# Kernel optimization log

Measured on AMD Instinct MI355X. Metric: run time of the kernel, lower is better.

Reference implementation:

```python
import jax, jax.numpy as jnp
import numpy as np

W_CE = 0.1
W_BOUND = 0.1
SMOOTH = 1e-06
IGNORE_INDEX = -100


def _edt_to_seeds(seed):
    """Exact Euclidean distance to nearest True pixel (Felzenszwalb-style separable EDT).

    seed: [H, W] bool. Returns [H, W] float32 distances (0 at seed pixels).
    Equivalent to scipy.ndimage.distance_transform_edt(~seed ... ) semantics:
    distance from every pixel to the nearest seed pixel.
    """
    H, W = seed.shape
    BIG = jnp.float32(H + W)  # upper bound on any in-image distance
    x = jnp.arange(W, dtype=jnp.float32)
    # 1D horizontal distance to nearest seed in the same row
    pos_l = jnp.where(seed, x, jnp.float32(-1e9))
    left = jax.lax.cummax(pos_l, axis=1)
    dl = x - left
    pos_r = jnp.where(seed, x, jnp.float32(1e9))
    right = jax.lax.cummin(pos_r, axis=1, reverse=True)
    dr = right - x
    d1 = jnp.minimum(jnp.minimum(dl, dr), BIG)  # [H, W], capped to avoid overflow
    g2 = d1 * d1  # squared horizontal distances
    # Vertical lower-envelope pass: dist2[y,x] = min_y' (y-y')^2 + g2[y',x]
    y = jnp.arange(H, dtype=jnp.float32)
    diff2 = (y[:, None] - y[None, :]) ** 2  # [H, H]
    dist2 = jnp.min(diff2[:, :, None] + g2[None, :, :], axis=1)  # [H, W]
    return jnp.sqrt(dist2)


def _signed_distance(class_mask):
    """signed = EDT(~mask) - EDT(mask) per scipy convention; 0 if mask empty."""
    has_pos = class_mask.any()
    has_neg = jnp.logical_not(class_mask).any()
    dist_out = _edt_to_seeds(class_mask)            # dist to nearest inside pixel (0 inside)
    dist_in = _edt_to_seeds(jnp.logical_not(class_mask))  # dist to nearest outside pixel (0 outside)
    signed = jnp.where(has_neg, dist_out - dist_in, dist_out)
    return jnp.where(has_pos, signed, jnp.zeros_like(signed))


def _dist_maps(targets, valid, num_classes):
    B, H, W = targets.shape
    t_safe = jnp.where(valid, targets, 0)
    cls = jnp.arange(num_classes, dtype=t_safe.dtype)
    cm = (t_safe[:, None, :, :] == cls[None, :, None, None]) & valid[:, None, :, :]  # [B,C,H,W]
    flat = cm.reshape(B * num_classes, H, W)
    signed = jax.lax.map(_signed_distance, flat).reshape(B, num_classes, H, W)
    return signed * valid[:, None, :, :].astype(jnp.float32)  # zero out invalid pixels


def setup_inputs() -> dict:
    key = jax.random.key(0)
    k1, k2 = jax.random.split(key)
    inputs = jax.random.normal(k1, (4, 8, 256, 256), dtype=jnp.float32)
    targets = jax.random.randint(k2, (4, 256, 256), 0, 8, dtype=jnp.int32)
    return {"inputs": inputs, "targets": targets}


def reference(inputs, targets):
    B, C, H, W = inputs.shape
    logp = jax.nn.log_softmax(inputs, axis=1)
    probs = jnp.exp(logp)
    # CrossEntropyLoss (all targets valid, mean over B*H*W)
    ce = -jnp.mean(jnp.take_along_axis(logp, targets[:, None, :, :].astype(jnp.int32), axis=1))
    # Dice loss (valid mask = targets >= 0)
    valid_d = targets >= 0
    t_safe = jnp.where(valid_d, targets, 0)
    onehot = jax.nn.one_hot(t_safe, C, dtype=jnp.float32).transpose(0, 3, 1, 2)  # [B,C,H,W]
    vm = valid_d[:, None, :, :].astype(jnp.float32)
    ps = probs * vm
    th = onehot * vm
    intersection = jnp.sum(ps * th)
    cardinality = jnp.sum(ps + th)
    dice = 1.0 - (2.0 * intersection + SMOOTH) / (cardinality + SMOOTH)
    dice_total = W_CE * ce + (1.0 - W_CE) * dice  # DiceCELoss.forward
    # Boundary loss (signed distance maps, mean reduction)
    valid_b = (targets != IGNORE_INDEX) & (targets >= 0) & (targets < C)
    dmaps = _dist_maps(targets, valid_b, C)
    vbf = valid_b[:, None, :, :].astype(jnp.float32)
    bound = jnp.sum(probs * dmaps * vbf) / (jnp.sum(vbf) + 1e-08)
    return W_CE * ce + (1.0 - W_CE - W_BOUND) * dice_total + W_BOUND * bound
```

## Files before the change

kernel.cpp:

```cpp
#include <hip/hip_runtime.h>
#include <math.h>

#define B_DIM 4
#define C_DIM 8
#define H_DIM 256
#define W_DIM 256
#define HW 65536
#define NPIX 262144


__device__ __forceinline__ float wave_reduce_f(float v) {
#pragma unroll
    for (int off = 32; off; off >>= 1) v += __shfl_xor(v, off, 64);
    return v;
}

__global__ void __launch_bounds__(256) k_row(
    const float* __restrict__ x, const int* __restrict__ tgt,
    float* __restrict__ lse_out, float* __restrict__ pce, float* __restrict__ pinter,
    int2* __restrict__ pcnt, unsigned long long* __restrict__ wmask_g,
    float* __restrict__ bound_part, unsigned int* __restrict__ cnt,
    unsigned int* __restrict__ gdone) {
    int bi = blockIdx.x;
    int b = bi >> 8, y = bi & 255;
    int i = threadIdx.x;
    int lane = i & 63, wid = i >> 6;
    size_t rowbase = (size_t)b * HW + (size_t)y * W_DIM;

    if (bi == 0) {
        if (i < 32) { bound_part[i << 5] = 0.0f; cnt[i << 5] = 0u; }
        if (i == 32) *gdone = 0u;
    }

    const float* xb = x + (size_t)b * C_DIM * HW + (size_t)y * W_DIM + i;
    float v[C_DIM];
    float m = -1e30f;
#pragma unroll
    for (int c = 0; c < C_DIM; ++c) { v[c] = xb[(size_t)c * HW]; m = fmaxf(m, v[c]); }
    float s = 0.f;
#pragma unroll
    for (int c = 0; c < C_DIM; ++c) s += __expf(v[c] - m);
    float lse = m + __logf(s);
    lse_out[rowbase + i] = lse;

    int t = tgt[rowbase + i];
    bool valid_d = (t >= 0);
    bool valid_b = valid_d && (t < C_DIM);
    int tc = valid_b ? t : 0;
    float vt = v[0];
#pragma unroll
    for (int c = 1; c < C_DIM; ++c) vt = (tc == c) ? v[c] : vt;

    float ce = lse - vt;
    float inter = valid_b ? __expf(vt - lse) : 0.f;

    __shared__ float ws_ce[4], ws_in[4];
    __shared__ int ws_cd[4], ws_cb[4];
    float r_ce = wave_reduce_f(ce);
    float r_in = wave_reduce_f(inter);
    unsigned long long md = __ballot(valid_d);
    unsigned long long mbv = __ballot(valid_b);
    if (lane == 0) {
        ws_ce[wid] = r_ce; ws_in[wid] = r_in;
        ws_cd[wid] = __popcll(md); ws_cb[wid] = __popcll(mbv);
    }

    __shared__ unsigned long long wmask[C_DIM][4];
#pragma unroll
    for (int c = 0; c < C_DIM; ++c) {
        unsigned long long mc = __ballot(valid_b && (t == c));
        if (lane == 0) wmask[c][wid] = mc;
    }
    __syncthreads();

    if (i == 0) {
        pce[bi] = (ws_ce[0] + ws_ce[1]) + (ws_ce[2] + ws_ce[3]);
        pinter[bi] = (ws_in[0] + ws_in[1]) + (ws_in[2] + ws_in[3]);
        pcnt[bi] = make_int2((ws_cd[0] + ws_cd[1]) + (ws_cd[2] + ws_cd[3]),
                             (ws_cb[0] + ws_cb[1]) + (ws_cb[2] + ws_cb[3]));
    }
    if (i < 32) {
        int c = i >> 2, w = i & 3;
        wmask_g[((size_t)((b * C_DIM + c) * 256 + y) << 2) + w] = wmask[c][w];
    }
}

#define LDS_PITCH 20
#define ENVELOPE(H, MA, MB)                                                     \
    {                                                                           \
        float4 qa0 = *(const float4*)&H[ybase][tx << 2];                        \
        float4 qb0 = *(const float4*)&H[ybase + 1][tx << 2];                    \
        MA.x = fminf(qa0.x, qb0.x + 1.0f); MB.x = fminf(qb0.x, qa0.x + 1.0f);   \
        MA.y = fminf(qa0.y, qb0.y + 1.0f); MB.y = fminf(qb0.y, qa0.y + 1.0f);   \
        MA.z = fminf(qa0.z, qb0.z + 1.0f); MB.z = fminf(qb0.z, qa0.z + 1.0f);   \
        MA.w = fminf(qa0.w, qb0.w + 1.0f); MB.w = fminf(qb0.w, qa0.w + 1.0f);   \
        int s = 1;                                                              \
        for (;;) {                                                              \
            int ra = max(ybase - s, 0);                                         \
            int rb = min(ybase + 1 + s, H_DIM - 1);                             \
            float4 qa = *(const float4*)&H[ra][tx << 2];                        \
            float4 qb = *(const float4*)&H[rb][tx << 2];                        \
            float s2a = (float)(s * s);                                         \
            float s2b = (float)((s + 1) * (s + 1));                             \
            MA.x = fminf(MA.x, fminf(qa.x + s2a, qb.x + s2b));                  \
            MA.y = fminf(MA.y, fminf(qa.y + s2a, qb.y + s2b));                  \
            MA.z = fminf(MA.z, fminf(qa.z + s2a, qb.z + s2b));                  \
            MA.w = fminf(MA.w, fminf(qa.w + s2a, qb.w + s2b));                  \
            MB.x = fminf(MB.x, fminf(qa.x + s2b, qb.x + s2a));                  \
            MB.y = fminf(MB.y, fminf(qa.y + s2b, qb.y + s2a));                  \
            MB.z = fminf(MB.z, fminf(qa.z + s2b, qb.z + s2a));                  \
            MB.w = fminf(MB.w, fminf(qa.w + s2b, qb.w + s2a));                  \
            float lmax = fmaxf(fmaxf(fmaxf(MA.x, MA.y), fmaxf(MA.z, MA.w)),     \
                               fmaxf(fmaxf(MB.x, MB.y), fmaxf(MB.z, MB.w)));    \
            ++s;                                                                \
            float st = (float)(s * s);                                          \
            if (s >= H_DIM || __all(st >= lmax)) break;                         \
        }                                                                       \
    }

__global__ void __launch_bounds__(512) k_cols(
    const unsigned long long* __restrict__ wmask_g, const float* __restrict__ x,
    const float* __restrict__ lse, const int* __restrict__ tgt,
    const float* __restrict__ pce, const float* __restrict__ pinter,
    const int2* __restrict__ pcnt,
    float* __restrict__ bound_part, unsigned int* __restrict__ cnt,
    unsigned int* __restrict__ gdone, float* __restrict__ out) {
    int blk = blockIdx.x;
    int bc = blk >> 4;
    int xt = blk & 15;
    int b = bc >> 3, c = bc & 7;
    int tid = threadIdx.x;
    int tx = tid & 3;
    int ybase = (tid >> 2) << 1;
    int lane = tid & 63, wid = tid >> 6;

    __shared__ float h0s[H_DIM][LDS_PITCH];
    __shared__ float h1s[H_DIM][LDS_PITCH];
    __shared__ int anyf[2];
    __shared__ float wsum[8];
    __shared__ int sh_last;
    __shared__ double dred[512];

    size_t pixbase = (size_t)b * HW;
    size_t xplane = ((size_t)b * C_DIM + c) * HW;
    int x0 = (xt << 4) + (tx << 2);
    size_t row0 = (size_t)ybase * W_DIM + x0;
    size_t row1 = row0 + W_DIM;
    float4 xv0 = *(const float4*)(x + xplane + row0);
    float4 xv1 = *(const float4*)(x + xplane + row1);
    float4 lv0 = *(const float4*)(lse + pixbase + row0);
    float4 lv1 = *(const float4*)(lse + pixbase + row1);
    int4 tv0 = *(const int4*)(tgt + pixbase + row0);
    int4 tv1 = *(const int4*)(tgt + pixbase + row1);

    int srow = tid & 255;
    int pol = tid >> 8;
    const unsigned long long* mrow = wmask_g + ((size_t)(bc * 256 + srow) << 2);
    unsigned long long w0 = mrow[0], w1 = mrow[1], w2 = mrow[2], w3 = mrow[3];

    if (tid < 2) anyf[tid] = 0;
    __syncthreads();
    if (pol == 0) {
        unsigned long long orv = w0 | w1 | w2 | w3;
        unsigned long long bp = __ballot(orv != 0ull);
        if (lane == 0 && bp) atomicOr(&anyf[0], 1);
    } else {
        unsigned long long andv = w0 & w1 & w2 & w3;
        unsigned long long bn = __ballot(andv != ~0ull);
        if (lane == 0 && bn) atomicOr(&anyf[1], 1);
    }

    {
        unsigned long long q0 = pol ? ~w0 : w0;
        unsigned long long q1 = pol ? ~w1 : w1;
        unsigned long long q2 = pol ? ~w2 : w2;
        unsigned long long q3 = pol ? ~w3 : w3;
        int wi = xt >> 2;
        int b0base = (xt & 3) << 4;
        int gc0 = xt << 4;
        int wbase = wi << 6;
        int h0p = q0 ? (63 - __builtin_clzll(q0)) : -100000;
        int h1p = q1 ? (127 - __builtin_clzll(q1)) : h0p;
        int h2p = q2 ? (191 - __builtin_clzll(q2)) : h1p;
        int lastp = (wi == 0) ? -100000 : (wi == 1) ? h0p : (wi == 2) ? h1p : h2p;
        int l3p = q3 ? (192 + __builtin_ctzll(q3)) : 100000;
        int l2p = q2 ? (128 + __builtin_ctzll(q2)) : l3p;
        int l1p = q1 ? (64 + __builtin_ctzll(q1)) : l2p;
        int nextp = (wi == 0) ? l1p : (wi == 1) ? l2p : (wi == 2) ? l3p : 100000;
        unsigned long long wn = (wi == 0) ? q0 : (wi == 1) ? q1 : (wi == 2) ? q2 : q3;
        unsigned long long lowmask = (b0base == 0) ? 0ull : ((~0ull) >> (64 - b0base));
        unsigned long long wlow = wn & lowmask;
        int lastw = wlow ? (wbase + 63 - __builtin_clzll(wlow)) : lastp;
        int hib = b0base + 16;
        unsigned long long whigh = (hib == 64) ? 0ull : (wn & ((~0ull) << hib));
        int nextw = whigh ? (wbase + __builtin_ctzll(whigh)) : nextp;
        unsigned int wseg = (unsigned int)((wn >> b0base) & 0xFFFFull);

        int d1l[16], d1r[16];
        int dl = gc0 - lastw;
#pragma unroll
        for (int i2 = 0; i2 < 16; ++i2) {
            dl = ((wseg >> i2) & 1u) ? 0 : dl;
            d1l[i2] = dl;
            ++dl;
        }
        int dr = nextw - (gc0 + 15);
#pragma unroll
        for (int i2 = 15; i2 >= 0; --i2) {
            dr = ((wseg >> i2) & 1u) ? 0 : dr;
            d1r[i2] = dr;
            ++dr;
        }
        float fd[16];
#pragma unroll
        for (int i2 = 0; i2 < 16; ++i2) {
            int d1 = min(min(d1l[i2], d1r[i2]), 512);
            fd[i2] = (float)d1 * (float)d1;
        }
        float (*hp)[LDS_PITCH] = pol ? h1s : h0s;
        *(float4*)&hp[srow][0]  = make_float4(fd[0], fd[1], fd[2], fd[3]);
        *(float4*)&hp[srow][4]  = make_float4(fd[4], fd[5], fd[6], fd[7]);
        *(float4*)&hp[srow][8]  = make_float4(fd[8], fd[9], fd[10], fd[11]);
        *(float4*)&hp[srow][12] = make_float4(fd[12], fd[13], fd[14], fd[15]);
    }
    __syncthreads();

    float4 m0a, m0b, m1a, m1b;
    ENVELOPE(h0s, m0a, m0b)
    ENVELOPE(h1s, m1a, m1b)

    bool has_pos = anyf[0] != 0;
    bool has_neg = anyf[1] != 0;

    float lsum = 0.f;
#pragma unroll
    for (int iy = 0; iy < 2; ++iy) {
        float4 M0 = iy ? m0b : m0a;
        float4 M1 = iy ? m1b : m1a;
        float4 xv = iy ? xv1 : xv0;
        float4 lv = iy ? lv1 : lv0;
        int4 tv = iy ? tv1 : tv0;
#pragma unroll
        for (int j = 0; j < 4; ++j) {
            float d2o = (j == 0) ? M0.x : (j == 1) ? M0.y : (j == 2) ? M0.z : M0.w;
            float d2i = (j == 0) ? M1.x : (j == 1) ? M1.y : (j == 2) ? M1.z : M1.w;
            float dout = sqrtf(d2o), din = sqrtf(d2i);
            float sgn = has_pos ? (has_neg ? (dout - din) : dout) : 0.f;
            float xs = (j == 0) ? xv.x : (j == 1) ? xv.y : (j == 2) ? xv.z : xv.w;
            float ls = (j == 0) ? lv.x : (j == 1) ? lv.y : (j == 2) ? lv.z : lv.w;
            int tt   = (j == 0) ? tv.x : (j == 1) ? tv.y : (j == 2) ? tv.z : tv.w;
            bool vb = (tt >= 0) && (tt < C_DIM);
            float prob = __expf(xs - ls);
            lsum += vb ? prob * sgn : 0.f;
        }
    }

    float r2 = wave_reduce_f(lsum);
    if (lane == 0) wsum[wid] = r2;
    __syncthreads();
    if (tid == 0) {
        float bsum = ((wsum[0] + wsum[1]) + (wsum[2] + wsum[3]))
                   + ((wsum[4] + wsum[5]) + (wsum[6] + wsum[7]));
        float old = atomicAdd(&bound_part[bc << 5], bsum);
        asm volatile("" :: "v"(old));
        unsigned int o = atomicAdd(&cnt[bc << 5], 1u);
        int lastflag = 0;
        if (o == 15u) {
            unsigned int g = atomicAdd(gdone, 1u);
            lastflag = (g == 31u) ? 1 : 0;
        }
        sh_last = lastflag;
    }
    __syncthreads();
    if (!sh_last) return;

    double s_ce = 0, s_in = 0, c_d = 0, c_b = 0;
    for (int k = tid; k < 1024; k += 512) {
        s_ce += (double)pce[k]; s_in += (double)pinter[k];
        int2 cc = pcnt[k]; c_d += (double)cc.x; c_b += (double)cc.y;
    }
    double sums[3]; double vin[3] = {s_ce, s_in, c_d * 4194304.0 + c_b};
    for (int q = 0; q < 3; ++q) {
        dred[tid] = vin[q];
        __syncthreads();
        for (int s2 = 256; s2; s2 >>= 1) { if (tid < s2) dred[tid] += dred[tid + s2]; __syncthreads(); }
        sums[q] = dred[0];
        __syncthreads();
    }
    __shared__ float bpart_s[32];
    if (tid < 32) bpart_s[tid] = atomicAdd(&bound_part[tid << 5], 0.0f);
    __syncthreads();
    if (tid == 0) {
        double btot = 0.0;
        for (int k = 0; k < 32; ++k) btot += (double)bpart_s[k];
        double packed = sums[2];
        double cd = floor(packed / 4194304.0 + 1e-9);
        double cb = packed - cd * 4194304.0;
        double ce = sums[0] / (double)NPIX;
        double inter = sums[1];
        double card = cd + cb;
        double dice = 1.0 - (2.0 * inter + 1e-6) / (card + 1e-6);
        double dice_total = 0.1 * ce + 0.9 * dice;
        double bound = btot / (cb + 1e-8);
        out[0] = (float)(0.1 * ce + 0.8 * dice_total + 0.1 * bound);
    }
}

extern "C" void kernel_launch(void* const* d_in, const int* in_sizes, int n_in,
                              void* d_out, int out_size, void* d_ws, size_t ws_size,
                              hipStream_t stream) {
    const float* x = (const float*)d_in[0];
    const int* tgt = (const int*)d_in[1];
    float* out = (float*)d_out;

    char* ws = (char*)d_ws;
    float* pce    = (float*)(ws + 0);
    float* pinter = (float*)(ws + 4096);
    int2*  pcnt   = (int2*)(ws + 8192);
    float* bound_part = (float*)(ws + 16384);
    unsigned int* cnt = (unsigned int*)(ws + 20480);
    unsigned int* gdone = (unsigned int*)(ws + 24576);
    float* lse    = (float*)(ws + 65536);
    unsigned long long* wmask_g = (unsigned long long*)(ws + (size_t)(2u << 20));

    k_row<<<1024, 256, 0, stream>>>(x, tgt, lse, pce, pinter, pcnt, wmask_g,
                                    bound_part, cnt, gdone);
    k_cols<<<512, 512, 0, stream>>>(wmask_g, x, lse, tgt, pce, pinter, pcnt,
                                    bound_part, cnt, gdone, out);
}
```

Baseline: 22.14 us.

## Narrow k_cols column tiles to 8 and fuse both EDT polarities per thread

k_cols now launches 1024 blocks of 256 threads, each covering 8 columns instead of 16. Each thread computes both the inside and outside horizontal distance rows, and the vertical envelope loop processes both polarities together with one shared early-exit vote. The aim is more blocks for better CU coverage and a single fused loop instead of two sequential envelope passes. The trade-off is that the fused loop runs to the slower polarity's termination, and per-block setup, mask loads and atomics are doubled.

```diff
diff --git a/kernel.cpp b/kernel.cpp
--- a/kernel.cpp
+++ b/kernel.cpp
@@ -85,40 +85,8 @@
     }
 }
 
-#define LDS_PITCH 20
-#define ENVELOPE(H, MA, MB)                                                     \
-    {                                                                           \
-        float4 qa0 = *(const float4*)&H[ybase][tx << 2];                        \
-        float4 qb0 = *(const float4*)&H[ybase + 1][tx << 2];                    \
-        MA.x = fminf(qa0.x, qb0.x + 1.0f); MB.x = fminf(qb0.x, qa0.x + 1.0f);   \
-        MA.y = fminf(qa0.y, qb0.y + 1.0f); MB.y = fminf(qb0.y, qa0.y + 1.0f);   \
-        MA.z = fminf(qa0.z, qb0.z + 1.0f); MB.z = fminf(qb0.z, qa0.z + 1.0f);   \
-        MA.w = fminf(qa0.w, qb0.w + 1.0f); MB.w = fminf(qb0.w, qa0.w + 1.0f);   \
-        int s = 1;                                                              \
-        for (;;) {                                                              \
-            int ra = max(ybase - s, 0);                                         \
-            int rb = min(ybase + 1 + s, H_DIM - 1);                             \
-            float4 qa = *(const float4*)&H[ra][tx << 2];                        \
-            float4 qb = *(const float4*)&H[rb][tx << 2];                        \
-            float s2a = (float)(s * s);                                         \
-            float s2b = (float)((s + 1) * (s + 1));                             \
-            MA.x = fminf(MA.x, fminf(qa.x + s2a, qb.x + s2b));                  \
-            MA.y = fminf(MA.y, fminf(qa.y + s2a, qb.y + s2b));                  \
-            MA.z = fminf(MA.z, fminf(qa.z + s2a, qb.z + s2b));                  \
-            MA.w = fminf(MA.w, fminf(qa.w + s2a, qb.w + s2b));                  \
-            MB.x = fminf(MB.x, fminf(qa.x + s2b, qb.x + s2a));                  \
-            MB.y = fminf(MB.y, fminf(qa.y + s2b, qb.y + s2a));                  \
-            MB.z = fminf(MB.z, fminf(qa.z + s2b, qb.z + s2a));                  \
-            MB.w = fminf(MB.w, fminf(qa.w + s2b, qb.w + s2a));                  \
-            float lmax = fmaxf(fmaxf(fmaxf(MA.x, MA.y), fmaxf(MA.z, MA.w)),     \
-                               fmaxf(fmaxf(MB.x, MB.y), fmaxf(MB.z, MB.w)));    \
-            ++s;                                                                \
-            float st = (float)(s * s);                                          \
-            if (s >= H_DIM || __all(st >= lmax)) break;                         \
-        }                                                                       \
-    }
-
-__global__ void __launch_bounds__(512) k_cols(
+#define LDS_PITCH 12
+__global__ void __launch_bounds__(256) k_cols(
     const unsigned long long* __restrict__ wmask_g, const float* __restrict__ x,
     const float* __restrict__ lse, const int* __restrict__ tgt,
     const float* __restrict__ pce, const float* __restrict__ pinter,
@@ -126,24 +94,24 @@
     float* __restrict__ bound_part, unsigned int* __restrict__ cnt,
     unsigned int* __restrict__ gdone, float* __restrict__ out) {
     int blk = blockIdx.x;
-    int bc = blk >> 4;
-    int xt = blk & 15;
+    int bc = blk >> 5;
+    int x8 = blk & 31;
     int b = bc >> 3, c = bc & 7;
     int tid = threadIdx.x;
-    int tx = tid & 3;
-    int ybase = (tid >> 2) << 1;
+    int tx = tid & 1;
+    int ybase = (tid >> 1) << 1;
     int lane = tid & 63, wid = tid >> 6;
 
     __shared__ float h0s[H_DIM][LDS_PITCH];
     __shared__ float h1s[H_DIM][LDS_PITCH];
     __shared__ int anyf[2];
-    __shared__ float wsum[8];
+    __shared__ float wsum[4];
     __shared__ int sh_last;
-    __shared__ double dred[512];
+    __shared__ double dred[256];
 
     size_t pixbase = (size_t)b * HW;
     size_t xplane = ((size_t)b * C_DIM + c) * HW;
-    int x0 = (xt << 4) + (tx << 2);
+    int x0 = (x8 << 3) + (tx << 2);
     size_t row0 = (size_t)ybase * W_DIM + x0;
     size_t row1 = row0 + W_DIM;
     float4 xv0 = *(const float4*)(x + xplane + row0);
@@ -153,81 +121,129 @@
     int4 tv0 = *(const int4*)(tgt + pixbase + row0);
     int4 tv1 = *(const int4*)(tgt + pixbase + row1);
 
-    int srow = tid & 255;
-    int pol = tid >> 8;
-    const unsigned long long* mrow = wmask_g + ((size_t)(bc * 256 + srow) << 2);
+    const unsigned long long* mrow = wmask_g + ((size_t)(bc * 256 + tid) << 2);
     unsigned long long w0 = mrow[0], w1 = mrow[1], w2 = mrow[2], w3 = mrow[3];
 
     if (tid < 2) anyf[tid] = 0;
     __syncthreads();
-    if (pol == 0) {
+    {
         unsigned long long orv = w0 | w1 | w2 | w3;
+        unsigned long long andv = w0 & w1 & w2 & w3;
         unsigned long long bp = __ballot(orv != 0ull);
-        if (lane == 0 && bp) atomicOr(&anyf[0], 1);
-    } else {
-        unsigned long long andv = w0 & w1 & w2 & w3;
         unsigned long long bn = __ballot(andv != ~0ull);
-        if (lane == 0 && bn) atomicOr(&anyf[1], 1);
+        if (lane == 0) {
+            if (bp) atomicOr(&anyf[0], 1);
+            if (bn) atomicOr(&anyf[1], 1);
+        }
     }
 
     {
-        unsigned long long q0 = pol ? ~w0 : w0;
-        unsigned long long q1 = pol ? ~w1 : w1;
-        unsigned long long q2 = pol ? ~w2 : w2;
-        unsigned long long q3 = pol ? ~w3 : w3;
-        int wi = xt >> 2;
-        int b0base = (xt & 3) << 4;
-        int gc0 = xt << 4;
+        int wi = x8 >> 3;
+        int b0base = (x8 & 7) << 3;
+        int gc0 = x8 << 3;
         int wbase = wi << 6;
-        int h0p = q0 ? (63 - __builtin_clzll(q0)) : -100000;
-        int h1p = q1 ? (127 - __builtin_clzll(q1)) : h0p;
-        int h2p = q2 ? (191 - __builtin_clzll(q2)) : h1p;
-        int lastp = (wi == 0) ? -100000 : (wi == 1) ? h0p : (wi == 2) ? h1p : h2p;
-        int l3p = q3 ? (192 + __builtin_ctzll(q3)) : 100000;
-        int l2p = q2 ? (128 + __builtin_ctzll(q2)) : l3p;
-        int l1p = q1 ? (64 + __builtin_ctzll(q1)) : l2p;
-        int nextp = (wi == 0) ? l1p : (wi == 1) ? l2p : (wi == 2) ? l3p : 100000;
-        unsigned long long wn = (wi == 0) ? q0 : (wi == 1) ? q1 : (wi == 2) ? q2 : q3;
-        unsigned long long lowmask = (b0base == 0) ? 0ull : ((~0ull) >> (64 - b0base));
-        unsigned long long wlow = wn & lowmask;
-        int lastw = wlow ? (wbase + 63 - __builtin_clzll(wlow)) : lastp;
-        int hib = b0base + 16;
-        unsigned long long whigh = (hib == 64) ? 0ull : (wn & ((~0ull) << hib));
-        int nextw = whigh ? (wbase + __builtin_ctzll(whigh)) : nextp;
-        unsigned int wseg = (unsigned int)((wn >> b0base) & 0xFFFFull);
-
-        int d1l[16], d1r[16];
-        int dl = gc0 - lastw;
-#pragma unroll
-        for (int i2 = 0; i2 < 16; ++i2) {
-            dl = ((wseg >> i2) & 1u) ? 0 : dl;
-            d1l[i2] = dl;
-            ++dl;
-        }
-        int dr = nextw - (gc0 + 15);
-#pragma unroll
-        for (int i2 = 15; i2 >= 0; --i2) {
-            dr = ((wseg >> i2) & 1u) ? 0 : dr;
-            d1r[i2] = dr;
-            ++dr;
-        }
-        float fd[16];
-#pragma unroll
-        for (int i2 = 0; i2 < 16; ++i2) {
-            int d1 = min(min(d1l[i2], d1r[i2]), 512);
-            fd[i2] = (float)d1 * (float)d1;
-        }
-        float (*hp)[LDS_PITCH] = pol ? h1s : h0s;
-        *(float4*)&hp[srow][0]  = make_float4(fd[0], fd[1], fd[2], fd[3]);
-        *(float4*)&hp[srow][4]  = make_float4(fd[4], fd[5], fd[6], fd[7]);
-        *(float4*)&hp[srow][8]  = make_float4(fd[8], fd[9], fd[10], fd[11]);
-        *(float4*)&hp[srow][12] = make_float4(fd[12], fd[13], fd[14], fd[15]);
+#pragma unroll
+        for (int pol = 0; pol < 2; ++pol) {
+            unsigned long long q0 = pol ? ~w0 : w0;
+            unsigned long long q1 = pol ? ~w1 : w1;
+            unsigned long long q2 = pol ? ~w2 : w2;
+            unsigned long long q3 = pol ? ~w3 : w3;
+            int h0p = q0 ? (63 - __builtin_clzll(q0)) : -100000;
+            int h1p = q1 ? (127 - __builtin_clzll(q1)) : h0p;
+            int h2p = q2 ? (191 - __builtin_clzll(q2)) : h1p;
+            int lastp = (wi == 0) ? -100000 : (wi == 1) ? h0p : (wi == 2) ? h1p : h2p;
+            int l3p = q3 ? (192 + __builtin_ctzll(q3)) : 100000;
+            int l2p = q2 ? (128 + __builtin_ctzll(q2)) : l3p;
+            int l1p = q1 ? (64 + __builtin_ctzll(q1)) : l2p;
+            int nextp = (wi == 0) ? l1p : (wi == 1) ? l2p : (wi == 2) ? l3p : 100000;
+            unsigned long long wn = (wi == 0) ? q0 : (wi == 1) ? q1 : (wi == 2) ? q2 : q3;
+            unsigned long long lowmask = (b0base == 0) ? 0ull : ((~0ull) >> (64 - b0base));
+            unsigned long long wlow = wn & lowmask;
+            int lastw = wlow ? (wbase + 63 - __builtin_clzll(wlow)) : lastp;
+            int hib = b0base + 8;
+            unsigned long long whigh = (hib == 64) ? 0ull : (wn & ((~0ull) << hib));
+            int nextw = whigh ? (wbase + __builtin_ctzll(whigh)) : nextp;
+            unsigned int wseg = (unsigned int)((wn >> b0base) & 0xFFull);
+
+            int d1l[8], d1r[8];
+            int dl = gc0 - lastw;
+#pragma unroll
+            for (int i2 = 0; i2 < 8; ++i2) {
+                dl = ((wseg >> i2) & 1u) ? 0 : dl;
+                d1l[i2] = dl;
+                ++dl;
+            }
+            int dr = nextw - (gc0 + 7);
+#pragma unroll
+            for (int i2 = 7; i2 >= 0; --i2) {
+                dr = ((wseg >> i2) & 1u) ? 0 : dr;
+                d1r[i2] = dr;
+                ++dr;
+            }
+            float fd[8];
+#pragma unroll
+            for (int i2 = 0; i2 < 8; ++i2) {
+                int d1 = min(min(d1l[i2], d1r[i2]), 512);
+                fd[i2] = (float)d1 * (float)d1;
+            }
+            float (*hp)[LDS_PITCH] = pol ? h1s : h0s;
+            *(float4*)&hp[tid][0] = make_float4(fd[0], fd[1], fd[2], fd[3]);
+            *(float4*)&hp[tid][4] = make_float4(fd[4], fd[5], fd[6], fd[7]);
+        }
     }
     __syncthreads();
 
     float4 m0a, m0b, m1a, m1b;
-    ENVELOPE(h0s, m0a, m0b)
-    ENVELOPE(h1s, m1a, m1b)
+    {
+        int col = tx << 2;
+        float4 a0 = *(const float4*)&h0s[ybase][col];
+        float4 b0v = *(const float4*)&h0s[ybase + 1][col];
+        float4 a1 = *(const float4*)&h1s[ybase][col];
+        float4 b1v = *(const float4*)&h1s[ybase + 1][col];
+        m0a.x = fminf(a0.x, b0v.x + 1.0f); m0b.x = fminf(b0v.x, a0.x + 1.0f);
+        m0a.y = fminf(a0.y, b0v.y + 1.0f); m0b.y = fminf(b0v.y, a0.y + 1.0f);
+        m0a.z = fminf(a0.z, b0v.z + 1.0f); m0b.z = fminf(b0v.z, a0.z + 1.0f);
+        m0a.w = fminf(a0.w, b0v.w + 1.0f); m0b.w = fminf(b0v.w, a0.w + 1.0f);
+        m1a.x = fminf(a1.x, b1v.x + 1.0f); m1b.x = fminf(b1v.x, a1.x + 1.0f);
+        m1a.y = fminf(a1.y, b1v.y + 1.0f); m1b.y = fminf(b1v.y, a1.y + 1.0f);
+        m1a.z = fminf(a1.z, b1v.z + 1.0f); m1b.z = fminf(b1v.z, a1.z + 1.0f);
+        m1a.w = fminf(a1.w, b1v.w + 1.0f); m1b.w = fminf(b1v.w, a1.w + 1.0f);
+        int s = 1;
+        for (;;) {
+            int ra = max(ybase - s, 0);
+            int rb = min(ybase + 1 + s, H_DIM - 1);
+            float4 qa0 = *(const float4*)&h0s[ra][col];
+            float4 qb0 = *(const float4*)&h0s[rb][col];
+            float4 qa1 = *(const float4*)&h1s[ra][col];
+            float4 qb1 = *(const float4*)&h1s[rb][col];
+            float s2a = (float)(s * s);
+            float s2b = (float)((s + 1) * (s + 1));
+            m0a.x = fminf(m0a.x, fminf(qa0.x + s2a, qb0.x + s2b));
+            m0a.y = fminf(m0a.y, fminf(qa0.y + s2a, qb0.y + s2b));
+            m0a.z = fminf(m0a.z, fminf(qa0.z + s2a, qb0.z + s2b));
+            m0a.w = fminf(m0a.w, fminf(qa0.w + s2a, qb0.w + s2b));
+            m0b.x = fminf(m0b.x, fminf(qa0.x + s2b, qb0.x + s2a));
+            m0b.y = fminf(m0b.y, fminf(qa0.y + s2b, qb0.y + s2a));
+            m0b.z = fminf(m0b.z, fminf(qa0.z + s2b, qb0.z + s2a));
+            m0b.w = fminf(m0b.w, fminf(qa0.w + s2b, qb0.w + s2a));
+            m1a.x = fminf(m1a.x, fminf(qa1.x + s2a, qb1.x + s2b));
+            m1a.y = fminf(m1a.y, fminf(qa1.y + s2a, qb1.y + s2b));
+            m1a.z = fminf(m1a.z, fminf(qa1.z + s2a, qb1.z + s2b));
+            m1a.w = fminf(m1a.w, fminf(qa1.w + s2a, qb1.w + s2b));
+            m1b.x = fminf(m1b.x, fminf(qa1.x + s2b, qb1.x + s2a));
+            m1b.y = fminf(m1b.y, fminf(qa1.y + s2b, qb1.y + s2a));
+            m1b.z = fminf(m1b.z, fminf(qa1.z + s2b, qb1.z + s2a));
+            m1b.w = fminf(m1b.w, fminf(qa1.w + s2b, qb1.w + s2a));
+            float l0 = fmaxf(fmaxf(fmaxf(m0a.x, m0a.y), fmaxf(m0a.z, m0a.w)),
+                             fmaxf(fmaxf(m0b.x, m0b.y), fmaxf(m0b.z, m0b.w)));
+            float l1 = fmaxf(fmaxf(fmaxf(m1a.x, m1a.y), fmaxf(m1a.z, m1a.w)),
+                             fmaxf(fmaxf(m1b.x, m1b.y), fmaxf(m1b.z, m1b.w)));
+            float lmax = fmaxf(l0, l1);
+            ++s;
+            float st = (float)(s * s);
+            if (s >= H_DIM || __all(st >= lmax)) break;
+        }
+    }
 
     bool has_pos = anyf[0] != 0;
     bool has_neg = anyf[1] != 0;
@@ -259,13 +275,12 @@
     if (lane == 0) wsum[wid] = r2;
     __syncthreads();
     if (tid == 0) {
-        float bsum = ((wsum[0] + wsum[1]) + (wsum[2] + wsum[3]))
-                   + ((wsum[4] + wsum[5]) + (wsum[6] + wsum[7]));
+        float bsum = (wsum[0] + wsum[1]) + (wsum[2] + wsum[3]);
         float old = atomicAdd(&bound_part[bc << 5], bsum);
         asm volatile("" :: "v"(old));
         unsigned int o = atomicAdd(&cnt[bc << 5], 1u);
         int lastflag = 0;
-        if (o == 15u) {
+        if (o == 31u) {
             unsigned int g = atomicAdd(gdone, 1u);
             lastflag = (g == 31u) ? 1 : 0;
         }
@@ -275,7 +290,7 @@
     if (!sh_last) return;
 
     double s_ce = 0, s_in = 0, c_d = 0, c_b = 0;
-    for (int k = tid; k < 1024; k += 512) {
+    for (int k = tid; k < 1024; k += 256) {
         s_ce += (double)pce[k]; s_in += (double)pinter[k];
         int2 cc = pcnt[k]; c_d += (double)cc.x; c_b += (double)cc.y;
     }
@@ -283,7 +298,7 @@
     for (int q = 0; q < 3; ++q) {
         dred[tid] = vin[q];
         __syncthreads();
-        for (int s2 = 256; s2; s2 >>= 1) { if (tid < s2) dred[tid] += dred[tid + s2]; __syncthreads(); }
+        for (int s2 = 128; s2; s2 >>= 1) { if (tid < s2) dred[tid] += dred[tid + s2]; __syncthreads(); }
         sums[q] = dred[0];
         __syncthreads();
     }
@@ -325,6 +340,6 @@
 
     k_row<<<1024, 256, 0, stream>>>(x, tgt, lse, pce, pinter, pcnt, wmask_g,
                                     bound_part, cnt, gdone);
-    k_cols<<<512, 512, 0, stream>>>(wmask_g, x, lse, tgt, pce, pinter, pcnt,
-                                    bound_part, cnt, gdone, out);
+    k_cols<<<1024, 256, 0, stream>>>(wmask_g, x, lse, tgt, pce, pinter, pcnt,
+                                     bound_part, cnt, gdone, out);
 }
```

New measurement: 26.35 us. 1.19x slower.
